# Optimization experiments

Hardware: AMD Instinct MI355X
Metric: run time of the kernel (lower is better)

The kernel has to match this reference:

```python
import jax, jax.numpy as jnp
import numpy as np

D_MODEL = 1024
H = 16
D_K = D_MODEL // H


def setup_inputs() -> dict:
    key = jax.random.key(0)
    ks = jax.random.split(key, 7)
    B, S = 4, 2048
    scale = 1.0 / np.sqrt(D_MODEL)
    return {
        "q": jax.random.normal(ks[0], (B, S, D_MODEL), dtype=jnp.float32),
        "k": jax.random.normal(ks[1], (B, S, D_MODEL), dtype=jnp.float32),
        "v": jax.random.normal(ks[2], (B, S, D_MODEL), dtype=jnp.float32),
        "W_q": jax.random.normal(ks[3], (D_MODEL, D_MODEL), dtype=jnp.float32) * scale,
        "W_k": jax.random.normal(ks[4], (D_MODEL, D_MODEL), dtype=jnp.float32) * scale,
        "W_v": jax.random.normal(ks[5], (D_MODEL, D_MODEL), dtype=jnp.float32) * scale,
        "W_o": jax.random.normal(ks[6], (D_MODEL, D_MODEL), dtype=jnp.float32) * scale,
    }


def reference(q, k, v, W_q, W_k, W_v, W_o):
    B, S, _ = q.shape
    # nn.Linear(bias=False): y = x @ W.T
    def proj(x, W):
        return (x @ W.T).reshape(B, -1, H, D_K).transpose(0, 2, 1, 3)  # [B,H,S,d_k]
    Q = proj(q, W_q)
    K = proj(k, W_k)
    V = proj(v, W_v)
    scores = jnp.einsum('bhqd,bhkd->bhqk', Q, K) / jnp.sqrt(jnp.float32(D_K))
    attn = jax.nn.softmax(scores, axis=-1)  # dropout p=0.0 -> identity
    ctx = jnp.einsum('bhqk,bhkd->bhqd', attn, V)
    ctx = ctx.transpose(0, 2, 1, 3).reshape(B, S, H * D_K)
    return ctx @ W_o.T
```

## Files before the change

kernel.cpp:

```cpp
#include <hip/hip_runtime.h>
#include <stdint.h>


typedef __attribute__((ext_vector_type(8))) short bf16x8;
typedef __attribute__((ext_vector_type(4))) float f32x4;

__device__ __forceinline__ void lds_async16(const void* g, void* l) {
  __builtin_amdgcn_global_load_lds(
      (const __attribute__((address_space(1))) void*)g,
      (__attribute__((address_space(3))) void*)l, 16, 0, 0);
}

__device__ __forceinline__ unsigned short f2bf(float f) {
  union { float f; unsigned u; } v; v.f = f;
  unsigned u = v.u + 0x7fffu + ((v.u >> 16) & 1u);
  return (unsigned short)(u >> 16);
}

__device__ __forceinline__ float fast_exp2(float x) {
#if __has_builtin(__builtin_amdgcn_exp2f)
  return __builtin_amdgcn_exp2f(x);
#else
  return exp2f(x);
#endif
}

__device__ __forceinline__ unsigned pk2(float a, float b) {
#if __has_builtin(__builtin_amdgcn_cvt_pk_bf16_f32)
  typedef __bf16 bf16v2 __attribute__((ext_vector_type(2)));
  union { bf16v2 v; unsigned u; } x;
  x.v = __builtin_amdgcn_cvt_pk_bf16_f32(a, b);
  return x.u;
#else
  return (unsigned)f2bf(a) | ((unsigned)f2bf(b) << 16);
#endif
}

__global__ void cvt_kernel(const float* s0, const float* s1, const float* s2, const float* s3,
                           unsigned short* d0, unsigned short* d1, unsigned short* d2, unsigned short* d3,
                           int n4) {
  int which = blockIdx.y;
  const float* s = which == 0 ? s0 : which == 1 ? s1 : which == 2 ? s2 : s3;
  unsigned short* d = which == 0 ? d0 : which == 1 ? d1 : which == 2 ? d2 : d3;
  int i = blockIdx.x * 256 + threadIdx.x;
  if (i < n4) {
    float4 v = ((const float4*)s)[i];
    ushort4 o;
    o.x = f2bf(v.x); o.y = f2bf(v.y); o.z = f2bf(v.z); o.w = f2bf(v.w);
    ((ushort4*)d)[i] = o;
  }
}

struct G256 { f32x4 acc[8][4]; };

__device__ __forceinline__ void stage_half256(const unsigned short* __restrict__ src,
                                              int rowbase, int kt, int h,
                                              unsigned short* lds, int tid) {
  const int srow = tid >> 3;
  const int g = tid & 7;
  const int col = ((g ^ (srow & 7)) << 3);
  const unsigned short* s0 = src + (size_t)(rowbase + h * 128 + srow) * 1024 + kt * 64 + col;
  char* d0 = (char*)lds + h * 16384 + tid * 16;
  lds_async16(s0, d0);
  lds_async16(s0 + (size_t)64 * 1024, d0 + 8192);
}

__device__ __forceinline__ void read_af(const unsigned short* buf, int wm, int c16, int q4,
                                        int ibase, bf16x8 (&af)[4][2]) {
#pragma unroll
  for (int ii = 0; ii < 4; ++ii)
#pragma unroll
    for (int ks = 0; ks < 2; ++ks) {
      int row = wm * 128 + (ibase + ii) * 16 + c16;
      af[ii][ks] = *(const bf16x8*)(buf + row * 64 + (((ks * 4 + q4) ^ (row & 7)) * 8));
    }
}

__device__ __forceinline__ void read_bf(const unsigned short* buf, int wn, int c16, int q4,
                                        int jbase, bf16x8 (&bf)[2][2]) {
#pragma unroll
  for (int jj = 0; jj < 2; ++jj)
#pragma unroll
    for (int ks = 0; ks < 2; ++ks) {
      int row = wn * 64 + (jbase + jj) * 16 + c16;
      bf[jj][ks] = *(const bf16x8*)(buf + row * 64 + (((ks * 4 + q4) ^ (row & 7)) * 8));
    }
}

__device__ __forceinline__ void mfma_quad(G256& G, const bf16x8 (&af)[4][2],
                                          const bf16x8 (&bf)[2][2], int i0, int j0) {
  __builtin_amdgcn_s_setprio(1);
#pragma unroll
  for (int ii = 0; ii < 4; ++ii)
#pragma unroll
    for (int jj = 0; jj < 2; ++jj)
#pragma unroll
      for (int ks = 0; ks < 2; ++ks)
        G.acc[i0 + ii][j0 + jj] = __builtin_amdgcn_mfma_f32_16x16x32_bf16(
            af[ii][ks], bf[jj][ks], G.acc[i0 + ii][j0 + jj], 0, 0, 0);
  __builtin_amdgcn_s_setprio(0);
}

__device__ __forceinline__ void gemm256_core(const unsigned short* __restrict__ A,
                                             const unsigned short* __restrict__ B,
                                             int tm, int tn,
                                             unsigned short* As0, unsigned short* As1,
                                             unsigned short* Bs0, unsigned short* Bs1,
                                             G256& G) {
  const int tid = threadIdx.x;
  const int lane = tid & 63;
  const int wv = tid >> 6;
  const int wm = wv >> 2, wn = wv & 3;
  const int c16 = lane & 15, q4 = lane >> 4;
  const int am = tm * 256, bn = tn * 256;

#pragma unroll
  for (int i = 0; i < 8; ++i)
#pragma unroll
    for (int j = 0; j < 4; ++j)
#pragma unroll
      for (int r = 0; r < 4; ++r) G.acc[i][j][r] = 0.f;

  stage_half256(B, bn, 0, 0, Bs0, tid);
  stage_half256(A, am, 0, 0, As0, tid);
  stage_half256(B, bn, 0, 1, Bs0, tid);
  stage_half256(A, am, 0, 1, As0, tid);
  stage_half256(B, bn, 1, 0, Bs1, tid);
  stage_half256(A, am, 1, 0, As1, tid);

  bf16x8 af[4][2], bfa[2][2], bfb[2][2];

  for (int i = 0; i < 8; ++i) {
    const int t1 = 2 * i + 1, t2 = 2 * i + 2, t3 = 2 * i + 3;
    const bool more = (i < 7);
    asm volatile("s_waitcnt vmcnt(4)" ::: "memory");
    __builtin_amdgcn_s_barrier();
    stage_half256(B, bn, t1, 1, Bs1, tid);
    read_af(As0, wm, c16, q4, 0, af);
    read_bf(Bs0, wn, c16, q4, 0, bfa);
    mfma_quad(G, af, bfa, 0, 0);
    __builtin_amdgcn_s_barrier();
    stage_half256(A, am, t1, 1, As1, tid);
    read_bf(Bs0, wn, c16, q4, 2, bfb);
    mfma_quad(G, af, bfb, 0, 2);
    __builtin_amdgcn_s_barrier();
    if (more) stage_half256(B, bn, t2, 0, Bs0, tid);
    read_af(As0, wm, c16, q4, 4, af);
    mfma_quad(G, af, bfb, 4, 2);
    __builtin_amdgcn_s_barrier();
    if (more) stage_half256(A, am, t2, 0, As0, tid);
    mfma_quad(G, af, bfa, 4, 0);
    if (more) { asm volatile("s_waitcnt vmcnt(4)" ::: "memory"); }
    else      { asm volatile("s_waitcnt vmcnt(0)" ::: "memory"); }
    __builtin_amdgcn_s_barrier();
    if (more) stage_half256(B, bn, t2, 1, Bs0, tid);
    read_af(As1, wm, c16, q4, 0, af);
    read_bf(Bs1, wn, c16, q4, 0, bfa);
    mfma_quad(G, af, bfa, 0, 0);
    __builtin_amdgcn_s_barrier();
    if (more) stage_half256(A, am, t2, 1, As0, tid);
    read_bf(Bs1, wn, c16, q4, 2, bfb);
    mfma_quad(G, af, bfb, 0, 2);
    __builtin_amdgcn_s_barrier();
    if (more) stage_half256(B, bn, t3, 0, Bs1, tid);
    read_af(As1, wm, c16, q4, 4, af);
    mfma_quad(G, af, bfb, 4, 2);
    __builtin_amdgcn_s_barrier();
    if (more) stage_half256(A, am, t3, 0, As1, tid);
    mfma_quad(G, af, bfa, 4, 0);
  }
}

__global__ __launch_bounds__(512, 2)
void qkv_kernel(const unsigned short* __restrict__ qb, const unsigned short* __restrict__ kb,
                const unsigned short* __restrict__ vb,
                const unsigned short* __restrict__ wq, const unsigned short* __restrict__ wk,
                const unsigned short* __restrict__ wv_,
                unsigned short* __restrict__ Qb, unsigned short* __restrict__ Kb,
                unsigned short* __restrict__ Vtb) {
  __shared__ unsigned short As0[256 * 64];
  __shared__ unsigned short As1[256 * 64];
  __shared__ unsigned short Bs0[256 * 64];
  __shared__ unsigned short Bs1[256 * 64];
  const int z = blockIdx.z;
  const unsigned short* A;
  const unsigned short* B;
  int tm, tn;
  if (z == 0)      { A = qb;  B = wq;  tm = blockIdx.y; tn = blockIdx.x; }
  else if (z == 1) { A = kb;  B = wk;  tm = blockIdx.y; tn = blockIdx.x; }
  else             { A = wv_; B = vb;  tm = blockIdx.x; tn = blockIdx.y; }

  G256 G;
  gemm256_core(A, B, tm, tn, As0, As1, Bs0, Bs1, G);

  const int lane = threadIdx.x & 63;
  const int wv = threadIdx.x >> 6;
  const int wm = wv >> 2, wn = wv & 3;
  const int c16 = lane & 15, q4 = lane >> 4;
  const float qscale = 0.125f * 1.44269504f;

#pragma unroll
  for (int i = 0; i < 8; ++i)
#pragma unroll
    for (int j = 0; j < 4; ++j)
#pragma unroll
      for (int r = 0; r < 4; ++r) {
        int m = tm * 256 + wm * 128 + i * 16 + q4 * 4 + r;
        int n = tn * 256 + wn * 64 + j * 16 + c16;
        float val = G.acc[i][j][r];
        if (z < 2) {
          if (z == 0) val *= qscale;
          int b = m >> 11, s_ = m & 2047, h = n >> 6, d = n & 63;
          unsigned short* dst = z == 0 ? Qb : Kb;
          dst[(((size_t)(b * 16 + h) * 2048 + s_) << 6) | d] = f2bf(val);
        } else {
          int h = m >> 6, d = m & 63, b = n >> 11, s_ = n & 2047;
          int sl = s_ & 127;
          int sp = (sl & ~31) | (((sl >> 2) & 3) << 3) | (((sl >> 4) & 1) << 2) | (sl & 3);
          s_ = (s_ & ~127) | sp;
          Vtb[((size_t)((b * 16 + h) * 64 + d) << 11) | s_] = f2bf(val);
        }
      }
}

__global__ __launch_bounds__(512, 2)
void out_gemm(const unsigned short* __restrict__ A, const unsigned short* __restrict__ B,
              float* __restrict__ C) {
  __shared__ unsigned short As0[256 * 64];
  __shared__ unsigned short As1[256 * 64];
  __shared__ unsigned short Bs0[256 * 64];
  __shared__ unsigned short Bs1[256 * 64];
  G256 G;
  gemm256_core(A, B, blockIdx.y, blockIdx.x, As0, As1, Bs0, Bs1, G);
  const int lane = threadIdx.x & 63;
  const int wv = threadIdx.x >> 6;
  const int wm = wv >> 2, wn = wv & 3;
  const int c16 = lane & 15, q4 = lane >> 4;
#pragma unroll
  for (int i = 0; i < 8; ++i)
#pragma unroll
    for (int j = 0; j < 4; ++j)
#pragma unroll
      for (int r = 0; r < 4; ++r) {
        int m = blockIdx.y * 256 + wm * 128 + i * 16 + q4 * 4 + r;
        int n = blockIdx.x * 256 + wn * 64 + j * 16 + c16;
        C[(size_t)m * 1024 + n] = G.acc[i][j][r];
      }
}

__global__ __launch_bounds__(128, 2)
void attn_kernel(const unsigned short* __restrict__ Q,
                 const unsigned short* __restrict__ K,
                 const unsigned short* __restrict__ Vt,
                 unsigned short* __restrict__ ctx) {
  __shared__ unsigned short Ks[2][64 * 64];
  __shared__ unsigned short Vs[2][64 * 64];

  const int tid = threadIdx.x, lane = tid & 63, w = tid >> 6;
  const int c16 = lane & 15, q4 = lane >> 4;
  const int wbase = w * 64;
  const unsigned wgid = blockIdx.x;
  const int bh = (int)((wgid & 7u) * 8 + ((wgid >> 3) & 7u));
  const int qt = (int)(wgid >> 6);
  const unsigned short* Qp = Q + ((size_t)bh * 2048 + qt * 128) * 64;
  const unsigned short* Kp = K + (size_t)bh * 2048 * 64;
  const unsigned short* Vp = Vt + (size_t)bh * 64 * 2048;

  const int srow = tid >> 3;
  const int gcol = (((tid & 7) ^ (srow & 7)) << 3);

  {
    const unsigned short* Qr = Qp + (size_t)srow * 64 + gcol;
    char* base = (char*)Ks + tid * 16;
#pragma unroll
    for (int c = 0; c < 8; ++c) lds_async16(Qr + c * 16 * 64, base + c * 2048);
  }
  __syncthreads();
  const unsigned short* Kflat = &Ks[0][0];
  bf16x8 qf[4][2];
#pragma unroll
  for (int nn = 0; nn < 4; ++nn)
#pragma unroll
    for (int ks = 0; ks < 2; ++ks) {
      int qr = wbase + nn * 16 + c16;
      int pos = (ks * 4 + q4) ^ (qr & 7);
      qf[nn][ks] = *(const bf16x8*)(Kflat + qr * 64 + pos * 8);
    }
  __syncthreads();

  bf16x8 onesf;
  {
    short v = (c16 == 0) ? (short)0x3F80 : (short)0;
#pragma unroll
    for (int j = 0; j < 8; ++j) onesf[j] = v;
  }

  f32x4 oacc[4][4];
  f32x4 lacc[4];
#pragma unroll
  for (int nn = 0; nn < 4; ++nn) {
#pragma unroll
    for (int r = 0; r < 4; ++r) lacc[nn][r] = 0.f;
#pragma unroll
    for (int dj = 0; dj < 4; ++dj)
#pragma unroll
      for (int r = 0; r < 4; ++r) oacc[nn][dj][r] = 0.f;
  }

  const unsigned short* Kr0 = Kp + (size_t)srow * 64 + gcol;
  const unsigned short* Vr0 = Vp + (size_t)srow * 2048 + gcol;

  {
    char* kb = (char*)Ks[0] + tid * 16;
    char* vb = (char*)Vs[0] + tid * 16;
#pragma unroll
    for (int c = 0; c < 4; ++c) {
      lds_async16(Kr0 + (size_t)c * 16 * 64, kb + c * 2048);
      lds_async16(Vr0 + (size_t)c * 16 * 2048, vb + c * 2048);
    }
  }

  int cur = 0;
  for (int kt = 0; kt < 32; ++kt) {
    __syncthreads();
    if (kt < 31) {
      char* kb = (char*)Ks[cur ^ 1] + tid * 16;
      char* vb = (char*)Vs[cur ^ 1] + tid * 16;
      const unsigned short* Krn = Kr0 + (size_t)(kt + 1) * 64 * 64;
      const unsigned short* Vrn = Vr0 + (size_t)(kt + 1) * 64;
#pragma unroll
      for (int c = 0; c < 4; ++c) {
        lds_async16(Krn + (size_t)c * 16 * 64, kb + c * 2048);
        lds_async16(Vrn + (size_t)c * 16 * 2048, vb + c * 2048);
      }
    }

    const unsigned short* KsC = Ks[cur];
    const unsigned short* VsC = Vs[cur];

#pragma unroll
    for (int ks2 = 0; ks2 < 2; ++ks2) {
      f32x4 s[2][4];
      __builtin_amdgcn_s_setprio(1);
#pragma unroll
      for (int ms = 0; ms < 2; ++ms) {
        const int row = (ks2 * 2 + ms) * 16 + c16;
        const bf16x8 kf0 = *(const bf16x8*)(KsC + row * 64 + ((0 + q4) ^ (row & 7)) * 8);
        const bf16x8 kf1 = *(const bf16x8*)(KsC + row * 64 + ((4 + q4) ^ (row & 7)) * 8);
#pragma unroll
        for (int nn = 0; nn < 4; ++nn) {
          f32x4 z = {0.f, 0.f, 0.f, 0.f};
          z = __builtin_amdgcn_mfma_f32_16x16x32_bf16(kf0, qf[nn][0], z, 0, 0, 0);
          z = __builtin_amdgcn_mfma_f32_16x16x32_bf16(kf1, qf[nn][1], z, 0, 0, 0);
          s[ms][nn] = z;
        }
      }
      __builtin_amdgcn_s_setprio(0);
      bf16x8 vf[4];
#pragma unroll
      for (int dj = 0; dj < 4; ++dj) {
        const int dr = dj * 16 + c16;
        vf[dj] = *(const bf16x8*)(VsC + dr * 64 + (((ks2 * 4 + q4) ^ (dr & 7))) * 8);
      }
      bf16x8 pfv[4];
#pragma unroll
      for (int nn = 0; nn < 4; ++nn) {
        union PU { unsigned u[4]; bf16x8 v; } pf;
        pf.u[0] = pk2(fast_exp2(s[0][nn][0]), fast_exp2(s[0][nn][1]));
        pf.u[1] = pk2(fast_exp2(s[0][nn][2]), fast_exp2(s[0][nn][3]));
        pf.u[2] = pk2(fast_exp2(s[1][nn][0]), fast_exp2(s[1][nn][1]));
        pf.u[3] = pk2(fast_exp2(s[1][nn][2]), fast_exp2(s[1][nn][3]));
        pfv[nn] = pf.v;
      }
      __builtin_amdgcn_s_setprio(1);
#pragma unroll
      for (int nn = 0; nn < 4; ++nn)
        lacc[nn] = __builtin_amdgcn_mfma_f32_16x16x32_bf16(pfv[nn], onesf, lacc[nn], 0, 0, 0);
#pragma unroll
      for (int dj = 0; dj < 4; ++dj)
#pragma unroll
        for (int nn = 0; nn < 4; ++nn)
          oacc[nn][dj] = __builtin_amdgcn_mfma_f32_16x16x32_bf16(pfv[nn], vf[dj], oacc[nn][dj], 0, 0, 0);
      __builtin_amdgcn_s_setprio(0);
    }
    cur ^= 1;
  }

  int b = bh >> 4, h = bh & 15;
#pragma unroll
  for (int nn = 0; nn < 4; ++nn)
#pragma unroll
    for (int r = 0; r < 4; ++r) {
      float l = __shfl(lacc[nn][r], lane & 48, 64);
      float inv = 1.f / l;
      int s_ = qt * 128 + wbase + nn * 16 + q4 * 4 + r;
#pragma unroll
      for (int dj = 0; dj < 4; ++dj) {
        int d = dj * 16 + c16;
        ctx[((size_t)(b * 2048 + s_)) * 1024 + h * 64 + d] = f2bf(oacc[nn][dj][r] * inv);
      }
    }
}

extern "C" void kernel_launch(void* const* d_in, const int* in_sizes, int n_in,
                              void* d_out, int out_size, void* d_ws, size_t ws_size,
                              hipStream_t stream) {
  const float* q  = (const float*)d_in[0];
  const float* k  = (const float*)d_in[1];
  const float* v  = (const float*)d_in[2];
  const float* Wq = (const float*)d_in[3];
  const float* Wk = (const float*)d_in[4];
  const float* Wv = (const float*)d_in[5];
  const float* Wo = (const float*)d_in[6];

  char* ws = (char*)d_ws;
  unsigned short* qb  = (unsigned short*)(ws);
  unsigned short* kb  = (unsigned short*)(ws + (16u << 20));
  unsigned short* vb  = (unsigned short*)(ws + (32u << 20));
  unsigned short* wqb = (unsigned short*)(ws + (48u << 20));
  unsigned short* wkb = (unsigned short*)(ws + (50u << 20));
  unsigned short* wvb = (unsigned short*)(ws + (52u << 20));
  unsigned short* wob = (unsigned short*)(ws + (54u << 20));
  unsigned short* Qb  = (unsigned short*)(ws + (56u << 20));
  unsigned short* Kb  = (unsigned short*)(ws + (72u << 20));
  unsigned short* Vtb = (unsigned short*)(ws + (88u << 20));
  unsigned short* ctxb = qb;

  cvt_kernel<<<dim3(1024, 4), 256, 0, stream>>>(Wq, Wk, Wv, Wo, wqb, wkb, wvb, wob, 262144);
  cvt_kernel<<<dim3(8192, 3), 256, 0, stream>>>(q, k, v, q, qb, kb, vb, qb, 2097152);

  qkv_kernel<<<dim3(4, 32, 3), 512, 0, stream>>>(qb, kb, vb, wqb, wkb, wvb, Qb, Kb, Vtb);

  attn_kernel<<<dim3(1024), 128, 0, stream>>>(Qb, Kb, Vtb, ctxb);

  out_gemm<<<dim3(4, 32), 512, 0, stream>>>(ctxb, wob, (float*)d_out);
}
```

Before: 354.7 us.

## Shrink GEMM M-tile to 128 rows to double block count

Changes the projection and output GEMMs from 256x256 to 128x256 tiles, halving the A LDS buffers and accumulators and reworking the staging/barrier schedule so each k-step loads one A half and two B halves. Grids double so the output GEMM fills more CUs and the QKV GEMM balances better. The trade is lower per-block arithmetic intensity, more redundant B traffic, and launch bounds that now allow only one block per CU.

```diff
diff --git a/kernel.cpp b/kernel.cpp
--- a/kernel.cpp
+++ b/kernel.cpp
@@ -51,11 +51,11 @@
   }
 }
 
-struct G256 { f32x4 acc[8][4]; };
-
-__device__ __forceinline__ void stage_half256(const unsigned short* __restrict__ src,
-                                              int rowbase, int kt, int h,
-                                              unsigned short* lds, int tid) {
+struct G256 { f32x4 acc[4][4]; };
+
+__device__ __forceinline__ void stage_half(const unsigned short* __restrict__ src,
+                                           int rowbase, int kt, int h,
+                                           unsigned short* lds, int tid) {
   const int srow = tid >> 3;
   const int g = tid & 7;
   const int col = ((g ^ (srow & 7)) << 3);
@@ -65,33 +65,22 @@
   lds_async16(s0 + (size_t)64 * 1024, d0 + 8192);
 }
 
-__device__ __forceinline__ void read_af(const unsigned short* buf, int wm, int c16, int q4,
-                                        int ibase, bf16x8 (&af)[4][2]) {
-#pragma unroll
-  for (int ii = 0; ii < 4; ++ii)
+__device__ __forceinline__ void read2(const unsigned short* buf, int rowbase, int c16, int q4,
+                                      int tbase, bf16x8 (&fr)[2][2]) {
+#pragma unroll
+  for (int tt = 0; tt < 2; ++tt)
 #pragma unroll
     for (int ks = 0; ks < 2; ++ks) {
-      int row = wm * 128 + (ibase + ii) * 16 + c16;
-      af[ii][ks] = *(const bf16x8*)(buf + row * 64 + (((ks * 4 + q4) ^ (row & 7)) * 8));
-    }
-}
-
-__device__ __forceinline__ void read_bf(const unsigned short* buf, int wn, int c16, int q4,
-                                        int jbase, bf16x8 (&bf)[2][2]) {
-#pragma unroll
-  for (int jj = 0; jj < 2; ++jj)
-#pragma unroll
-    for (int ks = 0; ks < 2; ++ks) {
-      int row = wn * 64 + (jbase + jj) * 16 + c16;
-      bf[jj][ks] = *(const bf16x8*)(buf + row * 64 + (((ks * 4 + q4) ^ (row & 7)) * 8));
-    }
-}
-
-__device__ __forceinline__ void mfma_quad(G256& G, const bf16x8 (&af)[4][2],
+      int row = rowbase + (tbase + tt) * 16 + c16;
+      fr[tt][ks] = *(const bf16x8*)(buf + row * 64 + (((ks * 4 + q4) ^ (row & 7)) * 8));
+    }
+}
+
+__device__ __forceinline__ void mfma_quad(G256& G, const bf16x8 (&af)[2][2],
                                           const bf16x8 (&bf)[2][2], int i0, int j0) {
   __builtin_amdgcn_s_setprio(1);
 #pragma unroll
-  for (int ii = 0; ii < 4; ++ii)
+  for (int ii = 0; ii < 2; ++ii)
 #pragma unroll
     for (int jj = 0; jj < 2; ++jj)
 #pragma unroll
@@ -110,76 +99,74 @@
   const int tid = threadIdx.x;
   const int lane = tid & 63;
   const int wv = tid >> 6;
-  const int wm = wv >> 2, wn = wv & 3;
+  const int wm = wv & 1, wn = wv >> 1;
   const int c16 = lane & 15, q4 = lane >> 4;
-  const int am = tm * 256, bn = tn * 256;
-
-#pragma unroll
-  for (int i = 0; i < 8; ++i)
+  const int am = tm * 128, bn = tn * 256;
+  const int arow = wm * 64, brow = wn * 64;
+
+#pragma unroll
+  for (int i = 0; i < 4; ++i)
 #pragma unroll
     for (int j = 0; j < 4; ++j)
 #pragma unroll
       for (int r = 0; r < 4; ++r) G.acc[i][j][r] = 0.f;
 
-  stage_half256(B, bn, 0, 0, Bs0, tid);
-  stage_half256(A, am, 0, 0, As0, tid);
-  stage_half256(B, bn, 0, 1, Bs0, tid);
-  stage_half256(A, am, 0, 1, As0, tid);
-  stage_half256(B, bn, 1, 0, Bs1, tid);
-  stage_half256(A, am, 1, 0, As1, tid);
-
-  bf16x8 af[4][2], bfa[2][2], bfb[2][2];
+  stage_half(B, bn, 0, 0, Bs0, tid);
+  stage_half(B, bn, 0, 1, Bs0, tid);
+  stage_half(A, am, 0, 0, As0, tid);
+  stage_half(B, bn, 1, 0, Bs1, tid);
+  stage_half(B, bn, 1, 1, Bs1, tid);
+
+  bf16x8 af[2][2], bfa[2][2], bfb[2][2];
 
   for (int i = 0; i < 8; ++i) {
     const int t1 = 2 * i + 1, t2 = 2 * i + 2, t3 = 2 * i + 3;
     const bool more = (i < 7);
     asm volatile("s_waitcnt vmcnt(4)" ::: "memory");
     __builtin_amdgcn_s_barrier();
-    stage_half256(B, bn, t1, 1, Bs1, tid);
-    read_af(As0, wm, c16, q4, 0, af);
-    read_bf(Bs0, wn, c16, q4, 0, bfa);
+    stage_half(A, am, t1, 0, As1, tid);
+    read2(As0, arow, c16, q4, 0, af);
+    read2(Bs0, brow, c16, q4, 0, bfa);
     mfma_quad(G, af, bfa, 0, 0);
     __builtin_amdgcn_s_barrier();
-    stage_half256(A, am, t1, 1, As1, tid);
-    read_bf(Bs0, wn, c16, q4, 2, bfb);
+    read2(Bs0, brow, c16, q4, 2, bfb);
     mfma_quad(G, af, bfb, 0, 2);
     __builtin_amdgcn_s_barrier();
-    if (more) stage_half256(B, bn, t2, 0, Bs0, tid);
-    read_af(As0, wm, c16, q4, 4, af);
-    mfma_quad(G, af, bfb, 4, 2);
-    __builtin_amdgcn_s_barrier();
-    if (more) stage_half256(A, am, t2, 0, As0, tid);
-    mfma_quad(G, af, bfa, 4, 0);
+    if (more) stage_half(B, bn, t2, 0, Bs0, tid);
+    read2(As0, arow, c16, q4, 2, af);
+    mfma_quad(G, af, bfb, 2, 2);
+    __builtin_amdgcn_s_barrier();
+    if (more) stage_half(B, bn, t2, 1, Bs0, tid);
+    mfma_quad(G, af, bfa, 2, 0);
     if (more) { asm volatile("s_waitcnt vmcnt(4)" ::: "memory"); }
     else      { asm volatile("s_waitcnt vmcnt(0)" ::: "memory"); }
     __builtin_amdgcn_s_barrier();
-    if (more) stage_half256(B, bn, t2, 1, Bs0, tid);
-    read_af(As1, wm, c16, q4, 0, af);
-    read_bf(Bs1, wn, c16, q4, 0, bfa);
+    if (more) stage_half(A, am, t2, 0, As0, tid);
+    read2(As1, arow, c16, q4, 0, af);
+    read2(Bs1, brow, c16, q4, 0, bfa);
     mfma_quad(G, af, bfa, 0, 0);
     __builtin_amdgcn_s_barrier();
-    if (more) stage_half256(A, am, t2, 1, As0, tid);
-    read_bf(Bs1, wn, c16, q4, 2, bfb);
+    read2(Bs1, brow, c16, q4, 2, bfb);
     mfma_quad(G, af, bfb, 0, 2);
     __builtin_amdgcn_s_barrier();
-    if (more) stage_half256(B, bn, t3, 0, Bs1, tid);
-    read_af(As1, wm, c16, q4, 4, af);
-    mfma_quad(G, af, bfb, 4, 2);
-    __builtin_amdgcn_s_barrier();
-    if (more) stage_half256(A, am, t3, 0, As1, tid);
-    mfma_quad(G, af, bfa, 4, 0);
-  }
-}
-
-__global__ __launch_bounds__(512, 2)
+    if (more) stage_half(B, bn, t3, 0, Bs1, tid);
+    read2(As1, arow, c16, q4, 2, af);
+    mfma_quad(G, af, bfb, 2, 2);
+    __builtin_amdgcn_s_barrier();
+    if (more) stage_half(B, bn, t3, 1, Bs1, tid);
+    mfma_quad(G, af, bfa, 2, 0);
+  }
+}
+
+__global__ __launch_bounds__(512, 1)
 void qkv_kernel(const unsigned short* __restrict__ qb, const unsigned short* __restrict__ kb,
                 const unsigned short* __restrict__ vb,
                 const unsigned short* __restrict__ wq, const unsigned short* __restrict__ wk,
                 const unsigned short* __restrict__ wv_,
                 unsigned short* __restrict__ Qb, unsigned short* __restrict__ Kb,
                 unsigned short* __restrict__ Vtb) {
-  __shared__ unsigned short As0[256 * 64];
-  __shared__ unsigned short As1[256 * 64];
+  __shared__ unsigned short As0[128 * 64];
+  __shared__ unsigned short As1[128 * 64];
   __shared__ unsigned short Bs0[256 * 64];
   __shared__ unsigned short Bs1[256 * 64];
   const int z = blockIdx.z;
@@ -188,24 +175,29 @@
   int tm, tn;
   if (z == 0)      { A = qb;  B = wq;  tm = blockIdx.y; tn = blockIdx.x; }
   else if (z == 1) { A = kb;  B = wk;  tm = blockIdx.y; tn = blockIdx.x; }
-  else             { A = wv_; B = vb;  tm = blockIdx.x; tn = blockIdx.y; }
+  else {
+    A = wv_; B = vb;
+    int idx = blockIdx.y * 4 + blockIdx.x;
+    tm = idx >> 5;
+    tn = idx & 31;
+  }
 
   G256 G;
   gemm256_core(A, B, tm, tn, As0, As1, Bs0, Bs1, G);
 
   const int lane = threadIdx.x & 63;
   const int wv = threadIdx.x >> 6;
-  const int wm = wv >> 2, wn = wv & 3;
+  const int wm = wv & 1, wn = wv >> 1;
   const int c16 = lane & 15, q4 = lane >> 4;
   const float qscale = 0.125f * 1.44269504f;
 
 #pragma unroll
-  for (int i = 0; i < 8; ++i)
+  for (int i = 0; i < 4; ++i)
 #pragma unroll
     for (int j = 0; j < 4; ++j)
 #pragma unroll
       for (int r = 0; r < 4; ++r) {
-        int m = tm * 256 + wm * 128 + i * 16 + q4 * 4 + r;
+        int m = tm * 128 + wm * 64 + i * 16 + q4 * 4 + r;
         int n = tn * 256 + wn * 64 + j * 16 + c16;
         float val = G.acc[i][j][r];
         if (z < 2) {
@@ -223,26 +215,26 @@
       }
 }
 
-__global__ __launch_bounds__(512, 2)
+__global__ __launch_bounds__(512, 1)
 void out_gemm(const unsigned short* __restrict__ A, const unsigned short* __restrict__ B,
               float* __restrict__ C) {
-  __shared__ unsigned short As0[256 * 64];
-  __shared__ unsigned short As1[256 * 64];
+  __shared__ unsigned short As0[128 * 64];
+  __shared__ unsigned short As1[128 * 64];
   __shared__ unsigned short Bs0[256 * 64];
   __shared__ unsigned short Bs1[256 * 64];
   G256 G;
   gemm256_core(A, B, blockIdx.y, blockIdx.x, As0, As1, Bs0, Bs1, G);
   const int lane = threadIdx.x & 63;
   const int wv = threadIdx.x >> 6;
-  const int wm = wv >> 2, wn = wv & 3;
+  const int wm = wv & 1, wn = wv >> 1;
   const int c16 = lane & 15, q4 = lane >> 4;
 #pragma unroll
-  for (int i = 0; i < 8; ++i)
+  for (int i = 0; i < 4; ++i)
 #pragma unroll
     for (int j = 0; j < 4; ++j)
 #pragma unroll
       for (int r = 0; r < 4; ++r) {
-        int m = blockIdx.y * 256 + wm * 128 + i * 16 + q4 * 4 + r;
+        int m = blockIdx.y * 128 + wm * 64 + i * 16 + q4 * 4 + r;
         int n = blockIdx.x * 256 + wn * 64 + j * 16 + c16;
         C[(size_t)m * 1024 + n] = G.acc[i][j][r];
       }
@@ -429,9 +421,9 @@
   cvt_kernel<<<dim3(1024, 4), 256, 0, stream>>>(Wq, Wk, Wv, Wo, wqb, wkb, wvb, wob, 262144);
   cvt_kernel<<<dim3(8192, 3), 256, 0, stream>>>(q, k, v, q, qb, kb, vb, qb, 2097152);
 
-  qkv_kernel<<<dim3(4, 32, 3), 512, 0, stream>>>(qb, kb, vb, wqb, wkb, wvb, Qb, Kb, Vtb);
+  qkv_kernel<<<dim3(4, 64, 3), 512, 0, stream>>>(qb, kb, vb, wqb, wkb, wvb, Qb, Kb, Vtb);
 
   attn_kernel<<<dim3(1024), 128, 0, stream>>>(Qb, Kb, Vtb, ctxb);
 
-  out_gemm<<<dim3(4, 32), 512, 0, stream>>>(ctxb, wob, (float*)d_out);
-}
+  out_gemm<<<dim3(4, 64), 512, 0, stream>>>(ctxb, wob, (float*)d_out);
+}
```

Result: faster. 324.9 us (-8.4%).
